# Performance work log

Hardware: AMD Instinct MI355X
Metric: run time of the kernel (lower is better)

Reference implementation:

```python
import jax, jax.numpy as jnp
import numpy as np

L, D, H, F, V, B, S = 4, 256, 8, 2048, 1024, 4, 1024
HD = D // H
EPS = 1e-5
PARAM_NAMES = ['enc_qkv_w','enc_qkv_b','enc_out_w','enc_out_b','enc_ff1_w','enc_ff1_b','enc_ff2_w','enc_ff2_b','enc_ln1_g','enc_ln1_b','enc_ln2_g','enc_ln2_b','dec_sa_qkv_w','dec_sa_qkv_b','dec_sa_out_w','dec_sa_out_b','dec_ca_qkv_w','dec_ca_qkv_b','dec_ca_out_w','dec_ca_out_b','dec_ff1_w','dec_ff1_b','dec_ff2_w','dec_ff2_b','dec_ln1_g','dec_ln1_b','dec_ln2_g','dec_ln2_b','dec_ln3_g','dec_ln3_b']

def _ln(x, g, b):
    m = jnp.mean(x, -1, keepdims=True)
    v = jnp.mean((x - m) ** 2, -1, keepdims=True)
    return (x - m) * jax.lax.rsqrt(v + EPS) * g + b

def _mha(q_in, kv_in, qkv_w, qkv_b, out_w, out_b, key_mask=None):
    wq, wk, wv = jnp.split(qkv_w, 3, axis=0)
    bq, bk, bv = jnp.split(qkv_b, 3, axis=0)
    q = (q_in @ wq.T + bq).reshape(q_in.shape[0], -1, H, HD)
    k = (kv_in @ wk.T + bk).reshape(kv_in.shape[0], -1, H, HD)
    v = (kv_in @ wv.T + bv).reshape(kv_in.shape[0], -1, H, HD)
    scores = jnp.einsum('bqhd,bkhd->bhqk', q, k) / np.float32(np.sqrt(HD))
    if key_mask is not None:
        scores = jnp.where(key_mask[:, None, None, :], jnp.float32(-1e9), scores)
    attn = jax.nn.softmax(scores, axis=-1)
    o = jnp.einsum('bhqk,bkhd->bqhd', attn, v).reshape(q_in.shape[0], -1, D)
    return o @ out_w.T + out_b

def _forward(x, mask, codebook, pos, p):
    h = codebook[x] + pos[:, :x.shape[1], :]  # [B,S,D]
    # --- bidirectional encoder (post-LN, ReLU FFN, torch defaults) ---
    ctx = h
    for l in range(L):
        sa = _mha(ctx, ctx, p['enc_qkv_w'][l], p['enc_qkv_b'][l], p['enc_out_w'][l], p['enc_out_b'][l], mask)
        ctx = _ln(ctx + sa, p['enc_ln1_g'][l], p['enc_ln1_b'][l])
        ff = jax.nn.relu(ctx @ p['enc_ff1_w'][l].T + p['enc_ff1_b'][l]) @ p['enc_ff2_w'][l].T + p['enc_ff2_b'][l]
        ctx = _ln(ctx + ff, p['enc_ln2_g'][l], p['enc_ln2_b'][l])
    # --- depth decoder: original loops per position with tgt len 1.
    # Self-attn over a single token == out_proj(v_proj(x)); cross-attn over the
    # shared context is independent per position, so all S positions batch exactly. ---
    d = h
    for l in range(L):
        wv = p['dec_sa_qkv_w'][l][2 * D:]
        bv = p['dec_sa_qkv_b'][l][2 * D:]
        sa = (d @ wv.T + bv) @ p['dec_sa_out_w'][l].T + p['dec_sa_out_b'][l]
        d = _ln(d + sa, p['dec_ln1_g'][l], p['dec_ln1_b'][l])
        ca = _mha(d, ctx, p['dec_ca_qkv_w'][l], p['dec_ca_qkv_b'][l], p['dec_ca_out_w'][l], p['dec_ca_out_b'][l])
        d = _ln(d + ca, p['dec_ln2_g'][l], p['dec_ln2_b'][l])
        ff = jax.nn.relu(d @ p['dec_ff1_w'][l].T + p['dec_ff1_b'][l]) @ p['dec_ff2_w'][l].T + p['dec_ff2_b'][l]
        d = _ln(d + ff, p['dec_ln3_g'][l], p['dec_ln3_b'][l])
    return d

def setup_inputs() -> dict:
    key = jax.random.key(0)
    ctr = [0]
    def nk():
        k = jax.random.fold_in(key, ctr[0]); ctr[0] += 1; return k
    def prm(shape):
        return jax.random.normal(nk(), shape, jnp.float32) * 0.02
    inp = {
        'x': jax.random.randint(nk(), (B, S), 0, V),
        'mask': jnp.zeros((B, S), bool),
        'codebook': prm((V, D)),
        'pos': prm((1, V, D)),
        'enc_qkv_w': prm((L, 3 * D, D)), 'enc_qkv_b': jnp.zeros((L, 3 * D)),
        'enc_out_w': prm((L, D, D)), 'enc_out_b': jnp.zeros((L, D)),
        'enc_ff1_w': prm((L, F, D)), 'enc_ff1_b': jnp.zeros((L, F)),
        'enc_ff2_w': prm((L, D, F)), 'enc_ff2_b': jnp.zeros((L, D)),
        'enc_ln1_g': jnp.ones((L, D)), 'enc_ln1_b': jnp.zeros((L, D)),
        'enc_ln2_g': jnp.ones((L, D)), 'enc_ln2_b': jnp.zeros((L, D)),
        'dec_sa_qkv_w': prm((L, 3 * D, D)), 'dec_sa_qkv_b': jnp.zeros((L, 3 * D)),
        'dec_sa_out_w': prm((L, D, D)), 'dec_sa_out_b': jnp.zeros((L, D)),
        'dec_ca_qkv_w': prm((L, 3 * D, D)), 'dec_ca_qkv_b': jnp.zeros((L, 3 * D)),
        'dec_ca_out_w': prm((L, D, D)), 'dec_ca_out_b': jnp.zeros((L, D)),
        'dec_ff1_w': prm((L, F, D)), 'dec_ff1_b': jnp.zeros((L, F)),
        'dec_ff2_w': prm((L, D, F)), 'dec_ff2_b': jnp.zeros((L, D)),
        'dec_ln1_g': jnp.ones((L, D)), 'dec_ln1_b': jnp.zeros((L, D)),
        'dec_ln2_g': jnp.ones((L, D)), 'dec_ln2_b': jnp.zeros((L, D)),
        'dec_ln3_g': jnp.ones((L, D)), 'dec_ln3_b': jnp.zeros((L, D)),
    }
    return inp

def reference(x, mask, codebook, pos, enc_qkv_w, enc_qkv_b, enc_out_w, enc_out_b, enc_ff1_w, enc_ff1_b, enc_ff2_w, enc_ff2_b, enc_ln1_g, enc_ln1_b, enc_ln2_g, enc_ln2_b, dec_sa_qkv_w, dec_sa_qkv_b, dec_sa_out_w, dec_sa_out_b, dec_ca_qkv_w, dec_ca_qkv_b, dec_ca_out_w, dec_ca_out_b, dec_ff1_w, dec_ff1_b, dec_ff2_w, dec_ff2_b, dec_ln1_g, dec_ln1_b, dec_ln2_g, dec_ln2_b, dec_ln3_g, dec_ln3_b):
    vals = (enc_qkv_w, enc_qkv_b, enc_out_w, enc_out_b, enc_ff1_w, enc_ff1_b, enc_ff2_w, enc_ff2_b, enc_ln1_g, enc_ln1_b, enc_ln2_g, enc_ln2_b, dec_sa_qkv_w, dec_sa_qkv_b, dec_sa_out_w, dec_sa_out_b, dec_ca_qkv_w, dec_ca_qkv_b, dec_ca_out_w, dec_ca_out_b, dec_ff1_w, dec_ff1_b, dec_ff2_w, dec_ff2_b, dec_ln1_g, dec_ln1_b, dec_ln2_g, dec_ln2_b, dec_ln3_g, dec_ln3_b)
    p = dict(zip(PARAM_NAMES, vals))
    return _forward(x, mask, codebook, pos, p)
```

## Files before the change

kernel.cpp:

```cpp
#include <hip/hip_runtime.h>

typedef unsigned short u16;
typedef unsigned int   u32;
typedef short short8 __attribute__((ext_vector_type(8)));
typedef float f32x4  __attribute__((ext_vector_type(4)));

#define DEV static __device__ __forceinline__

static constexpr int S_ = 1024;
static constexpr int D_ = 256;
static constexpr int NR = 4096;

DEV u16 f2bf(float x) {
    u32 u = __float_as_uint(x);
    return (u16)((u + 0x7FFFu + ((u >> 16) & 1u)) >> 16);
}
DEV float bf2f(u16 s) { return __uint_as_float(((u32)s) << 16); }


__global__ __launch_bounds__(256) void k_fillf(float* __restrict__ o, int n, float v) {
    int i = blockIdx.x * 256 + threadIdx.x;
    if (i < n) o[i] = v;
}

__global__ __launch_bounds__(256) void k_conv_all(
        const float* __restrict__ s0, const float* __restrict__ s1, const float* __restrict__ s2,
        const float* __restrict__ s3, const float* __restrict__ s4, const float* __restrict__ s5,
        const float* __restrict__ s6, const float* __restrict__ s7, const float* __restrict__ s8,
        const float* __restrict__ s9, u16* __restrict__ dst) {
    constexpr int c0 = 786432/4,            c1 = c0 + 262144/4,  c2 = c1 + 2097152/4,
                  c3 = c2 + 2097152/4,      c4 = c3 + 786432/4,  c5 = c4 + 262144/4,
                  c6 = c5 + 786432/4,       c7 = c6 + 262144/4,  c8 = c7 + 2097152/4,
                  c9 = c8 + 2097152/4;
    for (int i = blockIdx.x * 256 + threadIdx.x; i < c9; i += gridDim.x * 256) {
        const float* src; int base;
        if      (i < c0) { src = s0; base = 0;  }
        else if (i < c1) { src = s1; base = c0; }
        else if (i < c2) { src = s2; base = c1; }
        else if (i < c3) { src = s3; base = c2; }
        else if (i < c4) { src = s4; base = c3; }
        else if (i < c5) { src = s5; base = c4; }
        else if (i < c6) { src = s6; base = c5; }
        else if (i < c7) { src = s7; base = c6; }
        else if (i < c8) { src = s8; base = c7; }
        else             { src = s9; base = c8; }
        float4 v = ((const float4*)src)[i - base];
        ushort4 o; o.x = f2bf(v.x); o.y = f2bf(v.y); o.z = f2bf(v.z); o.w = f2bf(v.w);
        ((ushort4*)dst)[i] = o;
    }
}

__global__ __launch_bounds__(256) void k_wsa(const float* __restrict__ qkvw, const float* __restrict__ qkvb,
                                             const float* __restrict__ outw, const float* __restrict__ outb,
                                             u16* __restrict__ wsa, float* __restrict__ bsa) {
    int l = blockIdx.x >> 8, n = blockIdx.x & 255, t = threadIdx.x;
    const float* wv = qkvw + (size_t)l * 196608 + 131072;
    const float* bv = qkvb + l * 768 + 512;
    const float* wo = outw + (size_t)l * 65536 + n * 256;
    float acc = 0.0f, pb = 0.0f;
    for (int j = 0; j < 256; j++) {
        float woj = wo[j];
        acc = fmaf(woj, wv[j * 256 + t], acc);
        pb  = fmaf(woj, bv[j], pb);
    }
    wsa[(size_t)l * 65536 + n * 256 + t] = f2bf(acc);
    if (t == 0) bsa[l * 256 + n] = pb + outb[l * 256 + n];
}

__global__ __launch_bounds__(256) void k_embed(const int* __restrict__ xx,
                                               const float* __restrict__ cb,
                                               const float* __restrict__ pos,
                                               const unsigned char* __restrict__ mask,
                                               float* __restrict__ hf, u16* __restrict__ hb,
                                               float* __restrict__ av, float* __restrict__ avz) {
    int wid = threadIdx.x >> 6, lane = threadIdx.x & 63;
    int row = blockIdx.x * 4 + wid;
    int sp = row & (S_ - 1);
    int tok = xx[row];
    float4 c = ((const float4*)(cb + (size_t)tok * D_))[lane];
    float4 p = ((const float4*)(pos + (size_t)sp * D_))[lane];
    float4 s; s.x = c.x + p.x; s.y = c.y + p.y; s.z = c.z + p.z; s.w = c.w + p.w;
    ((float4*)(hf + (size_t)row * D_))[lane] = s;
    ushort4 o; o.x = f2bf(s.x); o.y = f2bf(s.y); o.z = f2bf(s.z); o.w = f2bf(s.w);
    ((ushort4*)(hb + (size_t)row * D_))[lane] = o;
    if (lane == 0) { av[row] = mask[row] ? -2.0e9f : 0.0f; avz[row] = 0.0f; }
}

__global__ __launch_bounds__(256) void k_ln(const float* __restrict__ x, const float* __restrict__ y,
                                            const float* __restrict__ gg, const float* __restrict__ bb,
                                            float* __restrict__ of, u16* __restrict__ ob) {
    int wid = threadIdx.x >> 6, lane = threadIdx.x & 63;
    int row = blockIdx.x * 4 + wid;
    float4 xv = ((const float4*)(x + (size_t)row * D_))[lane];
    float4 yv = ((const float4*)(y + (size_t)row * D_))[lane];
    float4 s; s.x = xv.x + yv.x; s.y = xv.y + yv.y; s.z = xv.z + yv.z; s.w = xv.w + yv.w;
    float sum = s.x + s.y + s.z + s.w;
    float sq  = s.x * s.x + s.y * s.y + s.z * s.z + s.w * s.w;
    #pragma unroll
    for (int m = 1; m < 64; m <<= 1) { sum += __shfl_xor(sum, m, 64); sq += __shfl_xor(sq, m, 64); }
    float mean = sum * (1.0f / 256.0f);
    float var  = sq * (1.0f / 256.0f) - mean * mean;
    float rs = rsqrtf(var + 1e-5f);
    float4 gv = ((const float4*)gg)[lane];
    float4 bv = ((const float4*)bb)[lane];
    float4 o;
    o.x = (s.x - mean) * rs * gv.x + bv.x;
    o.y = (s.y - mean) * rs * gv.y + bv.y;
    o.z = (s.z - mean) * rs * gv.z + bv.z;
    o.w = (s.w - mean) * rs * gv.w + bv.w;
    ((float4*)(of + (size_t)row * D_))[lane] = o;
    ushort4 ub; ub.x = f2bf(o.x); ub.y = f2bf(o.y); ub.z = f2bf(o.z); ub.w = f2bf(o.w);
    ((ushort4*)(ob + (size_t)row * D_))[lane] = ub;
}

__global__ __launch_bounds__(256) void k_ln4(const float* __restrict__ x, const u16* __restrict__ yp,
                                             const float* __restrict__ gg, const float* __restrict__ bb,
                                             float* __restrict__ of, u16* __restrict__ ob) {
    int wid = threadIdx.x >> 6, lane = threadIdx.x & 63;
    int row = blockIdx.x * 4 + wid;
    float4 xv = ((const float4*)(x + (size_t)row * D_))[lane];
    float4 s = xv;
    #pragma unroll
    for (int kz = 0; kz < 4; kz++) {
        ushort4 yv = ((const ushort4*)(yp + (size_t)kz * NR * D_ + (size_t)row * D_))[lane];
        s.x += bf2f(yv.x); s.y += bf2f(yv.y); s.z += bf2f(yv.z); s.w += bf2f(yv.w);
    }
    float sum = s.x + s.y + s.z + s.w;
    float sq  = s.x * s.x + s.y * s.y + s.z * s.z + s.w * s.w;
    #pragma unroll
    for (int m = 1; m < 64; m <<= 1) { sum += __shfl_xor(sum, m, 64); sq += __shfl_xor(sq, m, 64); }
    float mean = sum * (1.0f / 256.0f);
    float var  = sq * (1.0f / 256.0f) - mean * mean;
    float rs = rsqrtf(var + 1e-5f);
    float4 gv = ((const float4*)gg)[lane];
    float4 bv = ((const float4*)bb)[lane];
    float4 o;
    o.x = (s.x - mean) * rs * gv.x + bv.x;
    o.y = (s.y - mean) * rs * gv.y + bv.y;
    o.z = (s.z - mean) * rs * gv.z + bv.z;
    o.w = (s.w - mean) * rs * gv.w + bv.w;
    ((float4*)(of + (size_t)row * D_))[lane] = o;
    ushort4 ub; ub.x = f2bf(o.x); ub.y = f2bf(o.y); ub.z = f2bf(o.z); ub.w = f2bf(o.w);
    ((ushort4*)(ob + (size_t)row * D_))[lane] = ub;
}


template <int BM, int BN, bool RELU, bool OBF16>
__global__ __launch_bounds__(256) void k_gemm(const u16* __restrict__ A, const u16* __restrict__ Bw,
                                              const float* __restrict__ bias,
                                              float* __restrict__ Cf, u16* __restrict__ Cb,
                                              int Nn, int Kk) {
    constexpr int FM = BM / 32, FN = BN / 32;
    constexpr int LDA = 72;
    __shared__ __align__(16) u16 As[BM * LDA];
    __shared__ __align__(16) u16 Bs[BN * LDA];
    int tid = threadIdx.x, w = tid >> 6, lane = tid & 63;
    int lr = lane & 15, g = lane >> 4;
    int wm = w >> 1, wn = w & 1;
    int nbn = Nn / BN;
    int bid = blockIdx.x, nwg = gridDim.x;
    if ((nwg & 7) == 0) bid = (bid & 7) * (nwg >> 3) + (bid >> 3);
    int m0 = (bid / nbn) * BM, n0 = (bid % nbn) * BN;
    int trow = tid >> 3, tcol = (tid & 7) << 3;

    f32x4 acc[FM][FN] = {};

    for (int kb = 0; kb < Kk; kb += 64) {
        if (kb) __syncthreads();
        #pragma unroll
        for (int r = 0; r < BM / 32; r++) {
            int row = r * 32 + trow;
            uint4 v = *(const uint4*)(A + (size_t)(m0 + row) * Kk + kb + tcol);
            *(uint4*)(As + row * LDA + tcol) = v;
        }
        #pragma unroll
        for (int r = 0; r < BN / 32; r++) {
            int row = r * 32 + trow;
            uint4 v = *(const uint4*)(Bw + (size_t)(n0 + row) * Kk + kb + tcol);
            *(uint4*)(Bs + row * LDA + tcol) = v;
        }
        __syncthreads();
        #pragma unroll
        for (int kk = 0; kk < 2; kk++) {
            short8 af[FM], bfr[FN];
            #pragma unroll
            for (int mi = 0; mi < FM; mi++)
                af[mi] = *(const short8*)(As + (wm * (BM / 2) + mi * 16 + lr) * LDA + kk * 32 + g * 8);
            #pragma unroll
            for (int ni = 0; ni < FN; ni++)
                bfr[ni] = *(const short8*)(Bs + (wn * (BN / 2) + ni * 16 + lr) * LDA + kk * 32 + g * 8);
            #pragma unroll
            for (int mi = 0; mi < FM; mi++)
                #pragma unroll
                for (int ni = 0; ni < FN; ni++)
                    acc[mi][ni] = __builtin_amdgcn_mfma_f32_16x16x32_bf16(af[mi], bfr[ni], acc[mi][ni], 0, 0, 0);
        }
    }

    #pragma unroll
    for (int ni = 0; ni < FN; ni++) {
        int col = n0 + wn * (BN / 2) + ni * 16 + lr;
        float bi = bias[col];
        #pragma unroll
        for (int mi = 0; mi < FM; mi++) {
            #pragma unroll
            for (int jj = 0; jj < 4; jj++) {
                int row = m0 + wm * (BM / 2) + mi * 16 + g * 4 + jj;
                float v = acc[mi][ni][jj] + bi;
                if (RELU) v = fmaxf(v, 0.0f);
                if (OBF16) Cb[(size_t)row * Nn + col] = f2bf(v);
                else       Cf[(size_t)row * Nn + col] = v;
            }
        }
    }
}

__global__ __launch_bounds__(256) void k_gemm2(const u16* __restrict__ A0, const u16* __restrict__ W0,
                                               const float* __restrict__ b0, u16* __restrict__ C0,
                                               const u16* __restrict__ A1, const u16* __restrict__ W1,
                                               const float* __restrict__ b1, u16* __restrict__ C1) {
    constexpr int LDA = 72, Kk = 256;
    __shared__ __align__(16) u16 As[64 * LDA];
    __shared__ __align__(16) u16 Bs[64 * LDA];
    int tid = threadIdx.x, w = tid >> 6, lane = tid & 63;
    int lr = lane & 15, g = lane >> 4;
    int wm = w >> 1, wn = w & 1;
    int bid = blockIdx.x;
    bid = (bid & 7) * 96 + (bid >> 3);
    const u16 *A, *Bw; const float* bias; u16* Cb; int Nn, nbn, seg;
    if (bid < 256) { A = A0; Bw = W0; bias = b0; Cb = C0; Nn = 256; nbn = 4; seg = bid; }
    else           { A = A1; Bw = W1; bias = b1; Cb = C1; Nn = 512; nbn = 8; seg = bid - 256; }
    int m0 = (seg / nbn) * 64, n0 = (seg % nbn) * 64;
    int trow = tid >> 3, tcol = (tid & 7) << 3;

    f32x4 acc[2][2] = {};

    for (int kb = 0; kb < Kk; kb += 64) {
        if (kb) __syncthreads();
        #pragma unroll
        for (int r = 0; r < 2; r++) {
            int row = r * 32 + trow;
            uint4 va = *(const uint4*)(A + (size_t)(m0 + row) * Kk + kb + tcol);
            *(uint4*)(As + row * LDA + tcol) = va;
            uint4 vb = *(const uint4*)(Bw + (size_t)(n0 + row) * Kk + kb + tcol);
            *(uint4*)(Bs + row * LDA + tcol) = vb;
        }
        __syncthreads();
        #pragma unroll
        for (int kk = 0; kk < 2; kk++) {
            short8 af[2], bfr[2];
            #pragma unroll
            for (int mi = 0; mi < 2; mi++)
                af[mi] = *(const short8*)(As + (wm * 32 + mi * 16 + lr) * LDA + kk * 32 + g * 8);
            #pragma unroll
            for (int ni = 0; ni < 2; ni++)
                bfr[ni] = *(const short8*)(Bs + (wn * 32 + ni * 16 + lr) * LDA + kk * 32 + g * 8);
            #pragma unroll
            for (int mi = 0; mi < 2; mi++)
                #pragma unroll
                for (int ni = 0; ni < 2; ni++)
                    acc[mi][ni] = __builtin_amdgcn_mfma_f32_16x16x32_bf16(af[mi], bfr[ni], acc[mi][ni], 0, 0, 0);
        }
    }

    #pragma unroll
    for (int ni = 0; ni < 2; ni++) {
        int col = n0 + wn * 32 + ni * 16 + lr;
        float bi = bias[col];
        #pragma unroll
        for (int mi = 0; mi < 2; mi++)
            #pragma unroll
            for (int jj = 0; jj < 4; jj++) {
                int row = m0 + wm * 32 + mi * 16 + g * 4 + jj;
                Cb[(size_t)row * Nn + col] = f2bf(acc[mi][ni][jj] + bi);
            }
    }
}

__global__ __launch_bounds__(256) void k_gemm_sk4(const u16* __restrict__ A, const u16* __restrict__ Bw,
                                                  const float* __restrict__ bias, u16* __restrict__ Cp) {
    constexpr int LDA = 72, Nn = 256, Kk = 2048;
    __shared__ __align__(16) u16 As[64 * LDA];
    __shared__ __align__(16) u16 Bs[64 * LDA];
    int tid = threadIdx.x, w = tid >> 6, lane = tid & 63;
    int lr = lane & 15, g = lane >> 4;
    int wm = w >> 1, wn = w & 1;
    int kz = blockIdx.x >> 8;
    int mn = blockIdx.x & 255;
    mn = (mn & 7) * 32 + (mn >> 3);
    int m0 = (mn >> 2) * 64, n0 = (mn & 3) * 64;
    int kbeg = kz * 512;
    int trow = tid >> 3, tcol = (tid & 7) << 3;

    f32x4 acc[2][2] = {};

    for (int kb = kbeg; kb < kbeg + 512; kb += 64) {
        if (kb != kbeg) __syncthreads();
        #pragma unroll
        for (int r = 0; r < 2; r++) {
            int row = r * 32 + trow;
            uint4 va = *(const uint4*)(A + (size_t)(m0 + row) * Kk + kb + tcol);
            *(uint4*)(As + row * LDA + tcol) = va;
            uint4 vb = *(const uint4*)(Bw + (size_t)(n0 + row) * Kk + kb + tcol);
            *(uint4*)(Bs + row * LDA + tcol) = vb;
        }
        __syncthreads();
        #pragma unroll
        for (int kk = 0; kk < 2; kk++) {
            short8 af[2], bfr[2];
            #pragma unroll
            for (int mi = 0; mi < 2; mi++)
                af[mi] = *(const short8*)(As + (wm * 32 + mi * 16 + lr) * LDA + kk * 32 + g * 8);
            #pragma unroll
            for (int ni = 0; ni < 2; ni++)
                bfr[ni] = *(const short8*)(Bs + (wn * 32 + ni * 16 + lr) * LDA + kk * 32 + g * 8);
            #pragma unroll
            for (int mi = 0; mi < 2; mi++)
                #pragma unroll
                for (int ni = 0; ni < 2; ni++)
                    acc[mi][ni] = __builtin_amdgcn_mfma_f32_16x16x32_bf16(af[mi], bfr[ni], acc[mi][ni], 0, 0, 0);
        }
    }

    u16* Cz = Cp + (size_t)kz * NR * Nn;
    #pragma unroll
    for (int ni = 0; ni < 2; ni++) {
        int col = n0 + wn * 32 + ni * 16 + lr;
        float bi = (kz == 0) ? bias[col] : 0.0f;
        #pragma unroll
        for (int mi = 0; mi < 2; mi++)
            #pragma unroll
            for (int jj = 0; jj < 4; jj++) {
                int row = m0 + wm * 32 + mi * 16 + g * 4 + jj;
                Cz[(size_t)row * Nn + col] = f2bf(acc[mi][ni][jj] + bi);
            }
    }
}


__global__ __launch_bounds__(256) void k_attn(const u16* __restrict__ qp, int qs,
                                              const u16* __restrict__ kvp, int ks, int koff, int voff,
                                              const float* __restrict__ addv, u16* __restrict__ out) {
    __shared__ __align__(16) u16 Kl[2][128 * 32];
    __shared__ __align__(16) u16 VTl[2][32 * 136];
    __shared__ __align__(16) u16 Pl[4 * 16 * 136];
    __shared__ float Al[2][128];

    int tid = threadIdx.x, w = tid >> 6, lane = tid & 63;
    int lr = lane & 15, g = lane >> 4;
    int blk = blockIdx.x;
    blk = (blk & 7) * 64 + (blk >> 3);
    int qb = blk & 15, h = (blk >> 4) & 7, b = blk >> 7;
    int q0 = qb * 64 + w * 16;
    const float QS2 = 0.17677669529663687f * 1.4426950408889634f;

    short8 qf = *(const short8*)(qp + (size_t)(b * S_ + q0 + lr) * qs + h * 32 + g * 8);

    f32x4 o0 = {0.f, 0.f, 0.f, 0.f}, o1 = {0.f, 0.f, 0.f, 0.f};
    float m_run = -3.0e38f, l_run = 0.0f;
    float sreg[8][4];
    u16* Pw = Pl + w * 16 * 136;

    int key_t = tid >> 1, dh = (tid & 1) * 16;
    const u16* kbase = kvp + (size_t)(b * S_) * ks;

    uint4 ka0, ka1;
    union { uint4 v[2]; u16 s[16]; } vu;
    float alv = 0.0f;
    auto ldregs = [&](int kb) {
        const u16* srck = kbase + (size_t)(kb * 128 + key_t) * ks + koff + h * 32 + dh;
        ka0 = *(const uint4*)srck;
        ka1 = *(const uint4*)(srck + 8);
        const u16* srcv = kbase + (size_t)(kb * 128 + key_t) * ks + voff + h * 32 + dh;
        vu.v[0] = *(const uint4*)srcv;
        vu.v[1] = *(const uint4*)(srcv + 8);
        if (tid < 128) alv = addv[b * S_ + kb * 128 + tid];
    };
    auto stbuf = [&](int buf) {
        *(uint4*)(&Kl[buf][key_t * 32 + dh])     = ka0;
        *(uint4*)(&Kl[buf][key_t * 32 + dh + 8]) = ka1;
        #pragma unroll
        for (int i = 0; i < 16; i++) VTl[buf][(dh + i) * 136 + key_t] = vu.s[i];
        if (tid < 128) Al[buf][tid] = alv;
    };

    ldregs(0); stbuf(0);
    int cur = 0;
    for (int kb = 0; kb < 8; kb++) {
        __syncthreads();

        #pragma unroll
        for (int t = 0; t < 8; t++) {
            short8 kf = *(const short8*)(&Kl[cur][(t * 16 + lr) * 32 + g * 8]);
            f32x4 z = {0.f, 0.f, 0.f, 0.f};
            f32x4 st = __builtin_amdgcn_mfma_f32_16x16x32_bf16(kf, qf, z, 0, 0, 0);
            #pragma unroll
            for (int jj = 0; jj < 4; jj++) sreg[t][jj] = st[jj] * QS2 + Al[cur][t * 16 + g * 4 + jj];
        }

        if (kb < 7) ldregs(kb + 1);

        float mb = -3.0e38f;
        #pragma unroll
        for (int t = 0; t < 8; t++)
            #pragma unroll
            for (int jj = 0; jj < 4; jj++) mb = fmaxf(mb, sreg[t][jj]);
        mb = fmaxf(mb, __shfl_xor(mb, 16, 64));
        mb = fmaxf(mb, __shfl_xor(mb, 32, 64));
        float mnew = fmaxf(m_run, mb);
        float sc = __builtin_amdgcn_exp2f(m_run - mnew);
        float ls = 0.f;
        #pragma unroll
        for (int t = 0; t < 8; t++)
            #pragma unroll
            for (int jj = 0; jj < 4; jj++) {
                float p = __builtin_amdgcn_exp2f(sreg[t][jj] - mnew);
                sreg[t][jj] = p; ls += p;
            }
        ls += __shfl_xor(ls, 16, 64); ls += __shfl_xor(ls, 32, 64);
        l_run = l_run * sc + ls; m_run = mnew;
        #pragma unroll
        for (int jj = 0; jj < 4; jj++) {
            float scj = __shfl(sc, 20 * g + jj, 64);
            o0[jj] *= scj; o1[jj] *= scj;
        }

        #pragma unroll
        for (int t = 0; t < 8; t++) {
            u32 u0 = (u32)f2bf(sreg[t][0]) | ((u32)f2bf(sreg[t][1]) << 16);
            u32 u1 = (u32)f2bf(sreg[t][2]) | ((u32)f2bf(sreg[t][3]) << 16);
            *(uint2*)(Pw + lr * 136 + t * 16 + g * 4) = make_uint2(u0, u1);
        }

        #pragma unroll
        for (int c = 0; c < 4; c++) {
            short8 pa = *(const short8*)(Pw + lr * 136 + c * 32 + g * 8);
            short8 v0 = *(const short8*)(&VTl[cur][lr * 136 + c * 32 + g * 8]);
            short8 v1 = *(const short8*)(&VTl[cur][(16 + lr) * 136 + c * 32 + g * 8]);
            o0 = __builtin_amdgcn_mfma_f32_16x16x32_bf16(pa, v0, o0, 0, 0, 0);
            o1 = __builtin_amdgcn_mfma_f32_16x16x32_bf16(pa, v1, o1, 0, 0, 0);
        }

        __syncthreads();
        if (kb < 7) stbuf(cur ^ 1);
        cur ^= 1;
    }

    float li = 1.0f / l_run;
    #pragma unroll
    for (int jj = 0; jj < 4; jj++) {
        float lij = __shfl(li, 20 * g + jj, 64);
        int r = q0 + g * 4 + jj;
        u16* op = out + (size_t)(b * S_ + r) * 256 + h * 32;
        op[lr]      = f2bf(o0[jj] * lij);
        op[16 + lr] = f2bf(o1[jj] * lij);
    }
}


extern "C" void kernel_launch(void* const* d_in, const int* in_sizes, int n_in,
                              void* d_out, int out_size, void* d_ws, size_t ws_size,
                              hipStream_t stream) {
    const int* x                = (const int*)d_in[0];
    const unsigned char* mask   = (const unsigned char*)d_in[1];
    const float* codebook       = (const float*)d_in[2];
    const float* pos            = (const float*)d_in[3];
    const float* enc_qkv_w = (const float*)d_in[4];  const float* enc_qkv_b = (const float*)d_in[5];
    const float* enc_out_w = (const float*)d_in[6];  const float* enc_out_b = (const float*)d_in[7];
    const float* enc_ff1_w = (const float*)d_in[8];  const float* enc_ff1_b = (const float*)d_in[9];
    const float* enc_ff2_w = (const float*)d_in[10]; const float* enc_ff2_b = (const float*)d_in[11];
    const float* enc_ln1_g = (const float*)d_in[12]; const float* enc_ln1_b = (const float*)d_in[13];
    const float* enc_ln2_g = (const float*)d_in[14]; const float* enc_ln2_b = (const float*)d_in[15];
    const float* dec_sa_qkv_w = (const float*)d_in[16]; const float* dec_sa_qkv_b = (const float*)d_in[17];
    const float* dec_sa_out_w = (const float*)d_in[18]; const float* dec_sa_out_b = (const float*)d_in[19];
    const float* dec_ca_qkv_w = (const float*)d_in[20]; const float* dec_ca_qkv_b = (const float*)d_in[21];
    const float* dec_ca_out_w = (const float*)d_in[22]; const float* dec_ca_out_b = (const float*)d_in[23];
    const float* dec_ff1_w = (const float*)d_in[24]; const float* dec_ff1_b = (const float*)d_in[25];
    const float* dec_ff2_w = (const float*)d_in[26]; const float* dec_ff2_b = (const float*)d_in[27];
    const float* dec_ln1_g = (const float*)d_in[28]; const float* dec_ln1_b = (const float*)d_in[29];
    const float* dec_ln2_g = (const float*)d_in[30]; const float* dec_ln2_b = (const float*)d_in[31];
    const float* dec_ln3_g = (const float*)d_in[32]; const float* dec_ln3_b = (const float*)d_in[33];

    char* ws = (char*)d_ws; size_t off = 0;
    auto alloc = [&](size_t b) { char* p = ws + off; off += (b + 255) & ~(size_t)255; return p; };

    u16* w_eqkv  = (u16*)alloc((size_t)786432 * 2);
    u16* w_eout  = (u16*)alloc((size_t)262144 * 2);
    u16* w_eff1  = (u16*)alloc((size_t)2097152 * 2);
    u16* w_eff2  = (u16*)alloc((size_t)2097152 * 2);
    u16* w_dsaq  = (u16*)alloc((size_t)786432 * 2);
    u16* w_dsao  = (u16*)alloc((size_t)262144 * 2);
    u16* w_dcaq  = (u16*)alloc((size_t)786432 * 2);
    u16* w_dcao  = (u16*)alloc((size_t)262144 * 2);
    u16* w_dff1  = (u16*)alloc((size_t)2097152 * 2);
    u16* w_dff2  = (u16*)alloc((size_t)2097152 * 2);
    u16*   wsa   = (u16*)  alloc((size_t)4 * 65536 * 2);
    float* bsa   = (float*)alloc((size_t)4 * 256 * 4);
    float* h_f   = (float*)alloc((size_t)NR * D_ * 4);
    u16*   h_b   = (u16*)  alloc((size_t)NR * D_ * 2);
    float* ctx_f = (float*)alloc((size_t)NR * D_ * 4);
    u16*   ctx_b = (u16*)  alloc((size_t)NR * D_ * 2);
    float* dd_f  = (float*)alloc((size_t)NR * D_ * 4);
    u16*   dd_b  = (u16*)  alloc((size_t)NR * D_ * 2);
    float* gem_f = (float*)alloc((size_t)NR * 256 * 4);
    u16*   gem_p = (u16*)  alloc((size_t)4 * NR * 256 * 2);
    u16*   attno = (u16*)  alloc((size_t)NR * 256 * 2);
    float* addv  = (float*)alloc((size_t)NR * 4);
    float* addvz = (float*)alloc((size_t)NR * 4);
    u16* scr = (u16*)alloc((size_t)NR * 2048 * 2);
    u16* qkv_b = scr;
    u16* ffh_b = scr;
    u16* qca_b = scr;
    u16* kvca_b = scr + (size_t)NR * 256;
    (void)in_sizes; (void)n_in;

    if (off > ws_size) {
        k_fillf<<<(out_size + 255) / 256, 256, 0, stream>>>((float*)d_out, out_size, 1000.0f);
        return;
    }

    k_conv_all<<<2048, 256, 0, stream>>>(enc_qkv_w, enc_out_w, enc_ff1_w, enc_ff2_w,
                                         dec_sa_qkv_w, dec_sa_out_w, dec_ca_qkv_w, dec_ca_out_w,
                                         dec_ff1_w, dec_ff2_w, w_eqkv);
    k_wsa<<<1024, 256, 0, stream>>>(dec_sa_qkv_w, dec_sa_qkv_b, dec_sa_out_w, dec_sa_out_b, wsa, bsa);
    k_embed<<<1024, 256, 0, stream>>>(x, codebook, pos, mask, h_f, h_b, addv, addvz);

    for (int l = 0; l < 4; l++) {
        const u16* inb = l ? ctx_b : h_b;
        const float* inf = l ? ctx_f : h_f;
        k_gemm<64,64,false,true><<<768, 256, 0, stream>>>(inb, w_eqkv + (size_t)l*196608,
            enc_qkv_b + l*768, nullptr, qkv_b, 768, 256);
        k_attn<<<512, 256, 0, stream>>>(qkv_b, 768, qkv_b, 768, 256, 512, addv, attno);
        k_gemm<64,64,false,false><<<256, 256, 0, stream>>>(attno, w_eout + (size_t)l*65536,
            enc_out_b + l*256, gem_f, nullptr, 256, 256);
        k_ln<<<1024, 256, 0, stream>>>(inf, gem_f, enc_ln1_g + l*256, enc_ln1_b + l*256, ctx_f, ctx_b);
        k_gemm<128,128,true,true><<<512, 256, 0, stream>>>(ctx_b, w_eff1 + (size_t)l*524288,
            enc_ff1_b + l*2048, nullptr, ffh_b, 2048, 256);
        k_gemm_sk4<<<1024, 256, 0, stream>>>(ffh_b, w_eff2 + (size_t)l*524288,
            enc_ff2_b + l*256, gem_p);
        k_ln4<<<1024, 256, 0, stream>>>(ctx_f, gem_p, enc_ln2_g + l*256, enc_ln2_b + l*256, ctx_f, ctx_b);
    }

    for (int l = 0; l < 4; l++) {
        const u16* inb = l ? dd_b : h_b;
        const float* inf = l ? dd_f : h_f;
        k_gemm<64,64,false,false><<<256, 256, 0, stream>>>(inb, wsa + (size_t)l*65536,
            bsa + l*256, gem_f, nullptr, 256, 256);
        k_ln<<<1024, 256, 0, stream>>>(inf, gem_f, dec_ln1_g + l*256, dec_ln1_b + l*256, dd_f, dd_b);
        k_gemm2<<<768, 256, 0, stream>>>(dd_b, w_dcaq + (size_t)l*196608, dec_ca_qkv_b + l*768, qca_b,
                                         ctx_b, w_dcaq + (size_t)l*196608 + 65536,
                                         dec_ca_qkv_b + l*768 + 256, kvca_b);
        k_attn<<<512, 256, 0, stream>>>(qca_b, 256, kvca_b, 512, 0, 256, addvz, attno);
        k_gemm<64,64,false,false><<<256, 256, 0, stream>>>(attno, w_dcao + (size_t)l*65536,
            dec_ca_out_b + l*256, gem_f, nullptr, 256, 256);
        k_ln<<<1024, 256, 0, stream>>>(dd_f, gem_f, dec_ln2_g + l*256, dec_ln2_b + l*256, dd_f, dd_b);
        k_gemm<128,128,true,true><<<512, 256, 0, stream>>>(dd_b, w_dff1 + (size_t)l*524288,
            dec_ff1_b + l*2048, nullptr, ffh_b, 2048, 256);
        k_gemm_sk4<<<1024, 256, 0, stream>>>(ffh_b, w_dff2 + (size_t)l*524288,
            dec_ff2_b + l*256, gem_p);
        k_ln4<<<1024, 256, 0, stream>>>(dd_f, gem_p, dec_ln3_g + l*256, dec_ln3_b + l*256,
                                        (l == 3) ? (float*)d_out : dd_f, dd_b);
    }
}
```

Before: 601.3 us.

## Fuse 256-wide output projection GEMMs with residual add and LayerNorm

Adds a k_gemm_ln kernel in which each block computes a 16-row by 256-column tile of the projection GEMM, stages it through shared memory, then applies bias, the residual add and LayerNorm before writing fp32 and bf16 outputs. It replaces the separate GEMM and k_ln launches for the encoder out-projection and for the decoder self-attention and cross-attention out-projections, removing the fp32 intermediate buffer round trip and 12 launches. In exchange, every block reloads the full 256x256 weight tile into LDS while working on only 16 rows. That gives low arithmetic reuse per block, and the grid of 256 blocks leaves parallelism limited.

```diff
diff --git a/kernel.cpp b/kernel.cpp
--- a/kernel.cpp
+++ b/kernel.cpp
@@ -86,33 +86,6 @@
     if (lane == 0) { av[row] = mask[row] ? -2.0e9f : 0.0f; avz[row] = 0.0f; }
 }
 
-__global__ __launch_bounds__(256) void k_ln(const float* __restrict__ x, const float* __restrict__ y,
-                                            const float* __restrict__ gg, const float* __restrict__ bb,
-                                            float* __restrict__ of, u16* __restrict__ ob) {
-    int wid = threadIdx.x >> 6, lane = threadIdx.x & 63;
-    int row = blockIdx.x * 4 + wid;
-    float4 xv = ((const float4*)(x + (size_t)row * D_))[lane];
-    float4 yv = ((const float4*)(y + (size_t)row * D_))[lane];
-    float4 s; s.x = xv.x + yv.x; s.y = xv.y + yv.y; s.z = xv.z + yv.z; s.w = xv.w + yv.w;
-    float sum = s.x + s.y + s.z + s.w;
-    float sq  = s.x * s.x + s.y * s.y + s.z * s.z + s.w * s.w;
-    #pragma unroll
-    for (int m = 1; m < 64; m <<= 1) { sum += __shfl_xor(sum, m, 64); sq += __shfl_xor(sq, m, 64); }
-    float mean = sum * (1.0f / 256.0f);
-    float var  = sq * (1.0f / 256.0f) - mean * mean;
-    float rs = rsqrtf(var + 1e-5f);
-    float4 gv = ((const float4*)gg)[lane];
-    float4 bv = ((const float4*)bb)[lane];
-    float4 o;
-    o.x = (s.x - mean) * rs * gv.x + bv.x;
-    o.y = (s.y - mean) * rs * gv.y + bv.y;
-    o.z = (s.z - mean) * rs * gv.z + bv.z;
-    o.w = (s.w - mean) * rs * gv.w + bv.w;
-    ((float4*)(of + (size_t)row * D_))[lane] = o;
-    ushort4 ub; ub.x = f2bf(o.x); ub.y = f2bf(o.y); ub.z = f2bf(o.z); ub.w = f2bf(o.w);
-    ((ushort4*)(ob + (size_t)row * D_))[lane] = ub;
-}
-
 __global__ __launch_bounds__(256) void k_ln4(const float* __restrict__ x, const u16* __restrict__ yp,
                                              const float* __restrict__ gg, const float* __restrict__ bb,
                                              float* __restrict__ of, u16* __restrict__ ob) {
@@ -212,6 +185,94 @@
                 else       Cf[(size_t)row * Nn + col] = v;
             }
         }
+    }
+}
+
+__global__ __launch_bounds__(256) void k_gemm_ln(const u16* __restrict__ A, const u16* __restrict__ Bw,
+                                                 const float* __restrict__ bias,
+                                                 const float* __restrict__ resid,
+                                                 const float* __restrict__ gg, const float* __restrict__ bb,
+                                                 float* __restrict__ of, u16* __restrict__ ob) {
+    constexpr int LDA = 72, Kk = 256;
+    __shared__ __align__(16) u16 As[16 * LDA];
+    __shared__ __align__(16) u16 Bs[256 * LDA];
+    int tid = threadIdx.x, w = tid >> 6, lane = tid & 63;
+    int lr = lane & 15, g = lane >> 4;
+    int bid = blockIdx.x;
+    bid = (bid & 7) * 32 + (bid >> 3);
+    int m0 = bid * 16;
+    int trow = tid >> 3, tcol = (tid & 7) << 3;
+
+    f32x4 acc[4] = {};
+
+    for (int kb = 0; kb < Kk; kb += 64) {
+        if (kb) __syncthreads();
+        if (tid < 128) {
+            int row = tid >> 3;
+            uint4 v = *(const uint4*)(A + (size_t)(m0 + row) * Kk + kb + tcol);
+            *(uint4*)(As + row * LDA + tcol) = v;
+        }
+        #pragma unroll
+        for (int r = 0; r < 8; r++) {
+            int row = r * 32 + trow;
+            uint4 v = *(const uint4*)(Bw + (size_t)row * Kk + kb + tcol);
+            *(uint4*)(Bs + row * LDA + tcol) = v;
+        }
+        __syncthreads();
+        #pragma unroll
+        for (int kk = 0; kk < 2; kk++) {
+            short8 af = *(const short8*)(As + lr * LDA + kk * 32 + g * 8);
+            #pragma unroll
+            for (int ni = 0; ni < 4; ni++) {
+                short8 bfr = *(const short8*)(Bs + (w * 64 + ni * 16 + lr) * LDA + kk * 32 + g * 8);
+                acc[ni] = __builtin_amdgcn_mfma_f32_16x16x32_bf16(af, bfr, acc[ni], 0, 0, 0);
+            }
+        }
+    }
+
+    __syncthreads();
+    float* Cs = (float*)Bs;
+    #pragma unroll
+    for (int ni = 0; ni < 4; ni++) {
+        int col = w * 64 + ni * 16 + lr;
+        float bi = bias[col];
+        #pragma unroll
+        for (int jj = 0; jj < 4; jj++)
+            Cs[(g * 4 + jj) * 260 + col] = acc[ni][jj] + bi;
+    }
+    __syncthreads();
+
+    int row = tid >> 4, c0 = (tid & 15) * 16;
+    float v[16];
+    float sum = 0.0f, sq = 0.0f;
+    #pragma unroll
+    for (int i = 0; i < 4; i++) {
+        float4 cv = *(float4*)(Cs + row * 260 + c0 + i * 4);
+        float4 rv = *(const float4*)(resid + (size_t)(m0 + row) * D_ + c0 + i * 4);
+        v[4*i]   = cv.x + rv.x; v[4*i+1] = cv.y + rv.y;
+        v[4*i+2] = cv.z + rv.z; v[4*i+3] = cv.w + rv.w;
+    }
+    #pragma unroll
+    for (int i = 0; i < 16; i++) { sum += v[i]; sq += v[i] * v[i]; }
+    #pragma unroll
+    for (int m = 1; m < 16; m <<= 1) { sum += __shfl_xor(sum, m, 64); sq += __shfl_xor(sq, m, 64); }
+    float mean = sum * (1.0f / 256.0f);
+    float var  = sq * (1.0f / 256.0f) - mean * mean;
+    float rs = rsqrtf(var + 1e-5f);
+    float* op = of + (size_t)(m0 + row) * D_ + c0;
+    u16*   bp = ob + (size_t)(m0 + row) * D_ + c0;
+    #pragma unroll
+    for (int i = 0; i < 4; i++) {
+        float4 gv = *(const float4*)(gg + c0 + i * 4);
+        float4 bv = *(const float4*)(bb + c0 + i * 4);
+        float4 o;
+        o.x = (v[4*i]   - mean) * rs * gv.x + bv.x;
+        o.y = (v[4*i+1] - mean) * rs * gv.y + bv.y;
+        o.z = (v[4*i+2] - mean) * rs * gv.z + bv.z;
+        o.w = (v[4*i+3] - mean) * rs * gv.w + bv.w;
+        *(float4*)(op + i * 4) = o;
+        ushort4 ub; ub.x = f2bf(o.x); ub.y = f2bf(o.y); ub.z = f2bf(o.z); ub.w = f2bf(o.w);
+        *(ushort4*)(bp + i * 4) = ub;
     }
 }
 
@@ -502,7 +563,6 @@
     u16*   ctx_b = (u16*)  alloc((size_t)NR * D_ * 2);
     float* dd_f  = (float*)alloc((size_t)NR * D_ * 4);
     u16*   dd_b  = (u16*)  alloc((size_t)NR * D_ * 2);
-    float* gem_f = (float*)alloc((size_t)NR * 256 * 4);
     u16*   gem_p = (u16*)  alloc((size_t)4 * NR * 256 * 2);
     u16*   attno = (u16*)  alloc((size_t)NR * 256 * 2);
     float* addv  = (float*)alloc((size_t)NR * 4);
@@ -531,9 +591,8 @@
         k_gemm<64,64,false,true><<<768, 256, 0, stream>>>(inb, w_eqkv + (size_t)l*196608,
             enc_qkv_b + l*768, nullptr, qkv_b, 768, 256);
         k_attn<<<512, 256, 0, stream>>>(qkv_b, 768, qkv_b, 768, 256, 512, addv, attno);
-        k_gemm<64,64,false,false><<<256, 256, 0, stream>>>(attno, w_eout + (size_t)l*65536,
-            enc_out_b + l*256, gem_f, nullptr, 256, 256);
-        k_ln<<<1024, 256, 0, stream>>>(inf, gem_f, enc_ln1_g + l*256, enc_ln1_b + l*256, ctx_f, ctx_b);
+        k_gemm_ln<<<256, 256, 0, stream>>>(attno, w_eout + (size_t)l*65536, enc_out_b + l*256,
+            inf, enc_ln1_g + l*256, enc_ln1_b + l*256, ctx_f, ctx_b);
         k_gemm<128,128,true,true><<<512, 256, 0, stream>>>(ctx_b, w_eff1 + (size_t)l*524288,
             enc_ff1_b + l*2048, nullptr, ffh_b, 2048, 256);
         k_gemm_sk4<<<1024, 256, 0, stream>>>(ffh_b, w_eff2 + (size_t)l*524288,
@@ -544,16 +603,14 @@
     for (int l = 0; l < 4; l++) {
         const u16* inb = l ? dd_b : h_b;
         const float* inf = l ? dd_f : h_f;
-        k_gemm<64,64,false,false><<<256, 256, 0, stream>>>(inb, wsa + (size_t)l*65536,
-            bsa + l*256, gem_f, nullptr, 256, 256);
-        k_ln<<<1024, 256, 0, stream>>>(inf, gem_f, dec_ln1_g + l*256, dec_ln1_b + l*256, dd_f, dd_b);
+        k_gemm_ln<<<256, 256, 0, stream>>>(inb, wsa + (size_t)l*65536, bsa + l*256,
+            inf, dec_ln1_g + l*256, dec_ln1_b + l*256, dd_f, dd_b);
         k_gemm2<<<768, 256, 0, stream>>>(dd_b, w_dcaq + (size_t)l*196608, dec_ca_qkv_b + l*768, qca_b,
                                          ctx_b, w_dcaq + (size_t)l*196608 + 65536,
                                          dec_ca_qkv_b + l*768 + 256, kvca_b);
         k_attn<<<512, 256, 0, stream>>>(qca_b, 256, kvca_b, 512, 0, 256, addvz, attno);
-        k_gemm<64,64,false,false><<<256, 256, 0, stream>>>(attno, w_dcao + (size_t)l*65536,
-            dec_ca_out_b + l*256, gem_f, nullptr, 256, 256);
-        k_ln<<<1024, 256, 0, stream>>>(dd_f, gem_f, dec_ln2_g + l*256, dec_ln2_b + l*256, dd_f, dd_b);
+        k_gemm_ln<<<256, 256, 0, stream>>>(attno, w_dcao + (size_t)l*65536, dec_ca_out_b + l*256,
+            dd_f, dec_ln2_g + l*256, dec_ln2_b + l*256, dd_f, dd_b);
         k_gemm<128,128,true,true><<<512, 256, 0, stream>>>(dd_b, w_dff1 + (size_t)l*524288,
             dec_ff1_b + l*2048, nullptr, ffh_b, 2048, 256);
         k_gemm_sk4<<<1024, 256, 0, stream>>>(ffh_b, w_dff2 + (size_t)l*524288,
```

Result: faster. 579.6 us (-3.6%).
